# Optimization experiments

Hardware: AMD Instinct MI355X
Metric: run time of the kernel (lower is better)

Reference implementation:

```python
import jax, jax.numpy as jnp
import numpy as np

N, E, D, R, L, B, K = 10000, 160000, 256, 237, 6, 128, 33
EPS = 1e-6


def setup_inputs() -> dict:
    key = jax.random.key(0)
    ks = jax.random.split(key, 8)
    x = jax.random.uniform(ks[0], (N, D), dtype=jnp.float32)
    edge_index = jax.random.randint(ks[1], (2, E), 0, N)
    edge_type = jax.random.randint(ks[2], (E,), 0, R)
    batch = jax.random.randint(ks[3], (B, K, 3), 0, R)
    rel_embs = jax.random.normal(ks[4], (L, R, D), dtype=jnp.float32) * 0.02
    Ws = jax.random.normal(ks[5], (L, 13 * D, D), dtype=jnp.float32) * 0.02
    bs = jnp.zeros((L, D), dtype=jnp.float32)
    ln_scale = jnp.ones((L, D), dtype=jnp.float32)
    ln_bias = jnp.zeros((L, D), dtype=jnp.float32)
    relation_emb = jax.random.normal(ks[6], (R, D), dtype=jnp.float32) * 0.02
    return dict(x=x, rel_embs=rel_embs, Ws=Ws, bs=bs, ln_scale=ln_scale,
                ln_bias=ln_bias, relation_emb=relation_emb,
                edge_index=edge_index, edge_type=edge_type, batch=batch)


def _layer_norm(h, g, b, eps=1e-5):
    mu = jnp.mean(h, axis=-1, keepdims=True)
    var = jnp.var(h, axis=-1, keepdims=True)
    return (h - mu) * jax.lax.rsqrt(var + eps) * g + b


def _rgcn_conv(x, edge_index, edge_type, rel, W, b, g, be):
    # DistMult message + self-loop boundary, PNA aggregation, linear+LN+ReLU.
    n, d = x.shape
    src, dst = edge_index[0], edge_index[1]
    msg = x[src] * rel[edge_type]                       # [E, D]
    msg = jnp.concatenate([msg, x], axis=0)             # self-loop messages
    seg = jnp.concatenate([dst, jnp.arange(n)], axis=0)
    deg = jax.ops.segment_sum(jnp.ones((msg.shape[0],), jnp.float32), seg, n)  # >= 1
    inv_deg = 1.0 / deg[:, None]
    mean = jax.ops.segment_sum(msg, seg, n) * inv_deg
    sq_mean = jax.ops.segment_sum(msg * msg, seg, n) * inv_deg
    mx = jax.ops.segment_max(msg, seg, n)
    mn = jax.ops.segment_min(msg, seg, n)
    std = jnp.sqrt(jnp.clip(sq_mean - mean * mean, EPS))
    feats = jnp.concatenate([mean, mx, mn, std], axis=-1)          # [N, 4D]
    scale = jnp.log(deg)
    scale = scale / jnp.mean(scale)
    scales = jnp.stack([jnp.ones_like(scale), scale,
                        1.0 / jnp.clip(scale, 1e-2)], axis=-1)      # [N, 3]
    agg = (feats[:, :, None] * scales[:, None, :]).reshape(n, 12 * d)
    h = jnp.concatenate([agg, x], axis=-1) @ W + b                  # [N, D]
    return jax.nn.relu(_layer_norm(h, g, be))


def reference(x, rel_embs, Ws, bs, ln_scale, ln_bias, relation_emb,
              edge_index, edge_type, batch):
    for i in range(L):  # loop over layers (structurally distinct params)
        x = _rgcn_conv(x, edge_index, edge_type, rel_embs[i], Ws[i],
                       bs[i], ln_scale[i], ln_bias[i]) + x  # short_cut
    s = x[batch[:, :, 0]]                 # [B, K, D]
    r = relation_emb[batch[:, :, 1]]      # [B, K, D]
    t = x[batch[:, :, 2]]                 # [B, K, D]
    return jnp.sum(s * r * t, axis=-1)    # [B, K] DistMult scores
```

## Files before the change

kernel.cpp:

```cpp
#include <hip/hip_runtime.h>
#include <math.h>

typedef __attribute__((ext_vector_type(8))) _Float16 half8;
typedef __attribute__((ext_vector_type(4))) _Float16 half4;
typedef __attribute__((ext_vector_type(4))) float    floatx4;

#define N_NODES 10000
#define M_PAD   10112
#define MTILES  79
#define E_EDGES 160000
#define DIM     256
#define R_REL   237
#define L_LAYERS 6
#define B_BATCH 128
#define K_BATCH 33
#define K13     3328
#define KSPLIT  4
#define KSLICE  832
#define KS_STEPS 26
#define EPS_STD 1e-6f
#define EPS_LN  1e-5f

__device__ __forceinline__ void gload16(const void* g, void* lds) {
    __builtin_amdgcn_global_load_lds(
        (const __attribute__((address_space(1))) unsigned int*)g,
        (__attribute__((address_space(3))) unsigned int*)lds, 16, 0, 0);
}

__global__ void hist_kernel(const int* __restrict__ dst, int* __restrict__ deg) {
    int e = blockIdx.x * blockDim.x + threadIdx.x;
    if (e < E_EDGES) atomicAdd(&deg[dst[e]], 1);
}

__global__ void scan_kernel(const int* __restrict__ deg_in, int* __restrict__ offs,
                            int* __restrict__ cursor, float* __restrict__ sum_log) {
    __shared__ int   part[1024];
    __shared__ float slog[1024];
    int t = threadIdx.x;
    const int CH = 10;
    int base = t * CH;
    int lsum = 0; float ls = 0.f;
    for (int j = 0; j < CH; j++) {
        int i = base + j;
        if (i < N_NODES) { int d = deg_in[i]; lsum += d; ls += logf((float)(d + 1)); }
    }
    part[t] = lsum; slog[t] = ls;
    __syncthreads();
    for (int off = 1; off < 1024; off <<= 1) {
        int v = (t >= off) ? part[t - off] : 0;
        __syncthreads();
        part[t] += v;
        __syncthreads();
    }
    int run = part[t] - lsum;
    for (int j = 0; j < CH; j++) {
        int i = base + j;
        if (i < N_NODES) { offs[i] = run; cursor[i] = run; run += deg_in[i]; }
    }
    __syncthreads();
    for (int off = 512; off > 0; off >>= 1) {
        if (t < off) slog[t] += slog[t + off];
        __syncthreads();
    }
    if (t == 0) sum_log[0] = slog[0];
}

__global__ void fill_kernel(const int* __restrict__ src, const int* __restrict__ dst,
                            const int* __restrict__ et, int* __restrict__ cursor,
                            int* __restrict__ csr_src, int* __restrict__ csr_et) {
    int e = blockIdx.x * blockDim.x + threadIdx.x;
    if (e < E_EDGES) {
        int d = dst[e];
        int p = atomicAdd(&cursor[d], 1);
        csr_src[p] = src[e];
        csr_et[p]  = et[e];
    }
}

__global__ void scales_kernel(const int* __restrict__ deg_in, const float* __restrict__ sum_log,
                              float* __restrict__ s1, float* __restrict__ s2) {
    int i = blockIdx.x * blockDim.x + threadIdx.x;
    if (i < N_NODES) {
        float mean = sum_log[0] * (1.0f / (float)N_NODES);
        float sc = logf((float)(deg_in[i] + 1)) / mean;
        s1[i] = sc;
        s2[i] = 1.0f / fmaxf(sc, 0.01f);
    }
}

__global__ void wt_kernel(const float* __restrict__ Ws, _Float16* __restrict__ Wt) {
    int idx = blockIdx.x * 256 + threadIdx.x;
    const int TOT = L_LAYERS * 256 * K13;
    if (idx >= TOT) return;
    int l = idx / (256 * K13);
    int r = idx - l * (256 * K13);
    int n = r / K13, k = r - n * K13;
    int korig;
    if (k < 3072) {
        int t = k / 768;
        int rem = k - t * 768;
        int s = rem >> 8;
        int d = rem & 255;
        korig = (t * 256 + d) * 3 + s;
    } else {
        korig = k;
    }
    Wt[idx] = (_Float16)Ws[(size_t)l * K13 * 256 + (size_t)korig * 256 + n];
}

__global__ void cvt_kernel(const float* __restrict__ in, _Float16* __restrict__ outp, int n) {
    int i = blockIdx.x * 256 + threadIdx.x;
    if (i < n) outp[i] = (_Float16)in[i];
}

__global__ void agg_kernel(const float* __restrict__ x, const _Float16* __restrict__ xh,
                           const _Float16* __restrict__ relh,
                           const int* __restrict__ offs, const int* __restrict__ deg_in,
                           const int* __restrict__ csr_src, const int* __restrict__ csr_et,
                           _Float16* __restrict__ feats) {
    int wid  = threadIdx.x >> 6;
    int lane = threadIdx.x & 63;
    int node = blockIdx.x * 4 + wid;
    if (node >= N_NODES) return;
    int half = lane >> 5;
    int sub  = lane & 31;
    int off = offs[node];
    int end = off + deg_in[node];
    const half8* xh8 = (const half8*)xh;
    const half8* rh8 = (const half8*)relh;

    float s_[8], q_[8], mx_[8], mn_[8];
    #pragma unroll
    for (int i = 0; i < 8; i++) { s_[i] = 0.f; q_[i] = 0.f; mx_[i] = -INFINITY; mn_[i] = INFINITY; }

    for (int base = off; base < end; base += 2) {
        int e = base + half;
        if (e < end) {
            int sN = csr_src[e];
            int et = csr_et[e];
            half8 xv = xh8[(size_t)sN * 32 + sub];
            half8 rv = rh8[(size_t)et * 32 + sub];
            #pragma unroll
            for (int i = 0; i < 8; i++) {
                float m = (float)xv[i] * (float)rv[i];
                s_[i] += m; q_[i] += m * m;
                mx_[i] = fmaxf(mx_[i], m);
                mn_[i] = fminf(mn_[i], m);
            }
        }
    }
    #pragma unroll
    for (int i = 0; i < 8; i++) {
        s_[i] += __shfl_xor(s_[i], 32);
        q_[i] += __shfl_xor(q_[i], 32);
        mx_[i] = fmaxf(mx_[i], __shfl_xor(mx_[i], 32));
        mn_[i] = fminf(mn_[i], __shfl_xor(mn_[i], 32));
    }
    const float4* xrow = (const float4*)(x + (size_t)node * 256);
    float4 xa = xrow[sub * 2], xb = xrow[sub * 2 + 1];
    float xs[8] = {xa.x, xa.y, xa.z, xa.w, xb.x, xb.y, xb.z, xb.w};
    #pragma unroll
    for (int i = 0; i < 8; i++) {
        s_[i] += xs[i]; q_[i] += xs[i] * xs[i];
        mx_[i] = fmaxf(mx_[i], xs[i]);
        mn_[i] = fminf(mn_[i], xs[i]);
    }
    float inv = 1.0f / (float)(end - off + 1);
    half8 hm, hx, hn, hs;
    #pragma unroll
    for (int i = 0; i < 8; i++) {
        float mean = s_[i] * inv;
        float sd = sqrtf(fmaxf(q_[i] * inv - mean * mean, EPS_STD));
        hm[i] = (_Float16)mean; hx[i] = (_Float16)mx_[i];
        hn[i] = (_Float16)mn_[i]; hs[i] = (_Float16)sd;
    }
    half8* fout = (half8*)(feats + (size_t)node * 1024);
    if (half == 0) {
        fout[0 * 32 + sub] = hm;
        fout[1 * 32 + sub] = hx;
    } else {
        fout[2 * 32 + sub] = hn;
        fout[3 * 32 + sub] = hs;
    }
}

__launch_bounds__(256, 3)
__global__ void gemm_kernel(const _Float16* __restrict__ feats, const _Float16* __restrict__ xh,
                            const _Float16* __restrict__ Wt, const float* __restrict__ s1a,
                            const float* __restrict__ s2a, _Float16* __restrict__ hbuf) {
    __shared__ _Float16 sA[3][128 * 32];
    __shared__ _Float16 sB[3][128 * 32];

    int xcd = blockIdx.x & 7, loc = blockIdx.x >> 3;
    int lin = xcd * MTILES + loc;
    int ks  = lin / (2 * MTILES);
    int rem = lin - ks * (2 * MTILES);
    int nh  = rem / MTILES;
    int m   = rem - nh * MTILES;
    const int i0    = m * 128;
    const int n0    = nh * 128;
    const int kbase = ks * KSLICE;

    const int tid   = threadIdx.x;
    const int lane  = tid & 63;
    const int w     = tid >> 6;
    const int wr    = w >> 1;
    const int wc    = w & 1;
    const int row_l = lane & 15;
    const int kq    = lane >> 4;

    int a_off[4], b_off[4];
    #pragma unroll
    for (int rf = 0; rf < 4; rf++) {
        int r = wr * 64 + rf * 16 + row_l;
        a_off[rf] = r * 32 + ((kq ^ ((r >> 1) & 3)) & 3) * 8;
    }
    #pragma unroll
    for (int cf = 0; cf < 4; cf++) {
        int n_ = wc * 64 + cf * 16 + row_l;
        b_off[cf] = n_ * 32 + ((kq ^ ((n_ >> 1) & 3)) & 3) * 8;
    }

    const int arow = tid >> 2;
    const int ac   = tid & 3;
    const int aswz = ac ^ ((arow >> 1) & 3);
    const float s1lo = s1a[i0 + arow],      s2lo = s2a[i0 + arow];
    const float s1hi = s1a[i0 + arow + 64], s2hi = s2a[i0 + arow + 64];
    const _Float16* fb_lo = feats + (size_t)(i0 + arow) * 1024 + ac * 8;
    const _Float16* xb_lo = xh    + (size_t)(i0 + arow) * 256  + ac * 8;
    const _Float16* fb_hi = fb_lo + (size_t)64 * 1024;
    const _Float16* xb_hi = xb_lo + (size_t)64 * 256;

    const char* b_src[2];
    #pragma unroll
    for (int j = 0; j < 2; j++) {
        int rloc = j * 64 + w * 16 + (lane >> 2);
        int c = (lane & 3) ^ ((rloc >> 1) & 3);
        b_src[j] = (const char*)(Wt + (size_t)(n0 + rloc) * K13 + kbase + c * 8);
    }

    floatx4 acc[4][4];
    #pragma unroll
    for (int rf = 0; rf < 4; rf++)
        #pragma unroll
        for (int cf = 0; cf < 4; cf++)
            acc[rf][cf] = (floatx4){0.f, 0.f, 0.f, 0.f};

    half8 a0lo, a0hi, a1lo, a1hi, a2lo, a2hi;

#define A_OFS(S, OFS, SCL, SCH) do {                                          \
    int k0_ = kbase + (S) * 32;                                               \
    if (k0_ < 3072) {                                                         \
        int t_ = k0_ / 768;                                                   \
        int rem_ = k0_ - t_ * 768;                                            \
        int sI_ = rem_ >> 8;                                                  \
        OFS = t_ * 256 + (rem_ & 255);                                        \
        SCL = (sI_ == 0) ? 1.0f : (sI_ == 1 ? s1lo : s2lo);                   \
        SCH = (sI_ == 0) ? 1.0f : (sI_ == 1 ? s1hi : s2hi);                   \
    } else {                                                                  \
        OFS = -(k0_ - 3072) - 1;                                              \
        SCL = 1.0f; SCH = 1.0f;                                               \
    }                                                                         \
} while (0)

#define ALOAD(S, RLO, RHI) do {                                               \
    int ofs_; float scl_, sch_;                                               \
    A_OFS(S, ofs_, scl_, sch_);                                               \
    if (ofs_ >= 0) { RLO = *(const half8*)(fb_lo + ofs_);                     \
                     RHI = *(const half8*)(fb_hi + ofs_); }                   \
    else           { RLO = *(const half8*)(xb_lo + (-ofs_ - 1));              \
                     RHI = *(const half8*)(xb_hi + (-ofs_ - 1)); }            \
} while (0)

#define BSTAGE(BUF, S) do {                                                   \
    size_t koff_ = (size_t)(S) * 64;                                          \
    gload16(b_src[0] + koff_, (char*)(&sB[BUF][0]) + (0 * 64 + w * 16) * 64); \
    gload16(b_src[1] + koff_, (char*)(&sB[BUF][0]) + (1 * 64 + w * 16) * 64); \
} while (0)

#define AWRITE(BUF, S, RLO, RHI) do {                                         \
    int ofs_; float scl_, sch_;                                               \
    A_OFS(S, ofs_, scl_, sch_);                                               \
    half8 vl_ = RLO * (_Float16)scl_;                                         \
    half8 vh_ = RHI * (_Float16)sch_;                                         \
    *(half8*)(&sA[BUF][arow * 32 + aswz * 8]) = vl_;                          \
    *(half8*)(&sA[BUF][(arow + 64) * 32 + aswz * 8]) = vh_;                   \
} while (0)

#define COMPUTE(CB) do {                                                      \
    half8 af[4], bf[4];                                                       \
    _Pragma("unroll")                                                         \
    for (int rf = 0; rf < 4; rf++) af[rf] = *(const half8*)(&sA[CB][a_off[rf]]); \
    _Pragma("unroll")                                                         \
    for (int cf = 0; cf < 4; cf++) bf[cf] = *(const half8*)(&sB[CB][b_off[cf]]); \
    __builtin_amdgcn_s_setprio(1);                                            \
    _Pragma("unroll")                                                         \
    for (int rf = 0; rf < 4; rf++)                                            \
        _Pragma("unroll")                                                     \
        for (int cf = 0; cf < 4; cf++)                                        \
            acc[rf][cf] = __builtin_amdgcn_mfma_f32_16x16x32_f16(af[rf], bf[cf], acc[rf][cf], 0, 0, 0); \
    __builtin_amdgcn_s_setprio(0);                                            \
} while (0)

#define STEP(S, CBUF, ALO, AHI, NBUF, NLO, NHI) do {                          \
    asm volatile("s_waitcnt vmcnt(4)" ::: "memory");                          \
    AWRITE(CBUF, S, ALO, AHI);                                                \
    asm volatile("s_waitcnt lgkmcnt(0)" ::: "memory");                        \
    __builtin_amdgcn_sched_barrier(0);                                        \
    __builtin_amdgcn_s_barrier();                                             \
    ALOAD((S) + 2, NLO, NHI);                                                 \
    BSTAGE(NBUF, (S) + 2);                                                    \
    COMPUTE(CBUF);                                                            \
} while (0)

    ALOAD(0, a0lo, a0hi); BSTAGE(0, 0);
    ALOAD(1, a1lo, a1hi); BSTAGE(1, 1);

    int s = 0;
    for (int it = 0; it < 8; ++it, s += 3) {
        STEP(s + 0, 0, a0lo, a0hi, 2, a2lo, a2hi);
        STEP(s + 1, 1, a1lo, a1hi, 0, a0lo, a0hi);
        STEP(s + 2, 2, a2lo, a2hi, 1, a1lo, a1hi);
    }
    asm volatile("s_waitcnt vmcnt(4)" ::: "memory");
    AWRITE(0, 24, a0lo, a0hi);
    asm volatile("s_waitcnt lgkmcnt(0)" ::: "memory");
    __builtin_amdgcn_sched_barrier(0);
    __builtin_amdgcn_s_barrier();
    COMPUTE(0);
    asm volatile("s_waitcnt vmcnt(0)" ::: "memory");
    AWRITE(1, 25, a1lo, a1hi);
    asm volatile("s_waitcnt lgkmcnt(0)" ::: "memory");
    __builtin_amdgcn_sched_barrier(0);
    __builtin_amdgcn_s_barrier();
    COMPUTE(1);

#undef A_OFS
#undef ALOAD
#undef BSTAGE
#undef AWRITE
#undef COMPUTE
#undef STEP

    _Float16* outb = hbuf + (size_t)ks * M_PAD * 256;
    #pragma unroll
    for (int rf = 0; rf < 4; rf++) {
        #pragma unroll
        for (int j = 0; j < 4; j++) {
            int grow = i0 + wr * 64 + rf * 16 + kq * 4 + j;
            _Float16* orow = outb + (size_t)grow * 256 + n0 + wc * 64;
            #pragma unroll
            for (int cf = 0; cf < 4; cf++)
                orow[cf * 16 + row_l] = (_Float16)acc[rf][cf][j];
        }
    }
}

__global__ void ln_kernel(const _Float16* __restrict__ hbuf, const float* __restrict__ xin,
                          const float* __restrict__ bvec, const float* __restrict__ gvec,
                          const float* __restrict__ evec, float* __restrict__ xout,
                          _Float16* __restrict__ xhout) {
    int wid = threadIdx.x >> 6, lane = threadIdx.x & 63;
    int row = blockIdx.x * 4 + wid;
    if (row >= N_NODES) return;
    const half4* p0 = (const half4*)(hbuf + (size_t)row * 256);
    const half4* p1 = (const half4*)(hbuf + (size_t)M_PAD * 256     + (size_t)row * 256);
    const half4* p2 = (const half4*)(hbuf + (size_t)M_PAD * 256 * 2 + (size_t)row * 256);
    const half4* p3 = (const half4*)(hbuf + (size_t)M_PAD * 256 * 3 + (size_t)row * 256);
    half4 h0 = p0[lane], h1 = p1[lane], h2 = p2[lane], h3 = p3[lane];
    float4 bv = ((const float4*)bvec)[lane];
    float4 hv;
    hv.x = (float)h0.x + (float)h1.x + (float)h2.x + (float)h3.x + bv.x;
    hv.y = (float)h0.y + (float)h1.y + (float)h2.y + (float)h3.y + bv.y;
    hv.z = (float)h0.z + (float)h1.z + (float)h2.z + (float)h3.z + bv.z;
    hv.w = (float)h0.w + (float)h1.w + (float)h2.w + (float)h3.w + bv.w;
    float s = hv.x + hv.y + hv.z + hv.w;
    float qsq = hv.x*hv.x + hv.y*hv.y + hv.z*hv.z + hv.w*hv.w;
    #pragma unroll
    for (int off = 1; off < 64; off <<= 1) {
        s   += __shfl_xor(s, off);
        qsq += __shfl_xor(qsq, off);
    }
    float mu  = s * (1.0f / 256.0f);
    float var = qsq * (1.0f / 256.0f) - mu * mu;
    float rs  = rsqrtf(var + EPS_LN);
    float4 g = ((const float4*)gvec)[lane];
    float4 e = ((const float4*)evec)[lane];
    float4 xv = ((const float4*)(xin + (size_t)row * 256))[lane];
    float4 o;
    o.x = fmaxf((hv.x - mu) * rs * g.x + e.x, 0.f) + xv.x;
    o.y = fmaxf((hv.y - mu) * rs * g.y + e.y, 0.f) + xv.y;
    o.z = fmaxf((hv.z - mu) * rs * g.z + e.z, 0.f) + xv.z;
    o.w = fmaxf((hv.w - mu) * rs * g.w + e.w, 0.f) + xv.w;
    ((float4*)(xout + (size_t)row * 256))[lane] = o;
    half4 oh = { (_Float16)o.x, (_Float16)o.y, (_Float16)o.z, (_Float16)o.w };
    ((half4*)(xhout + (size_t)row * 256))[lane] = oh;
}

__global__ void score_kernel(const float* __restrict__ x, const float* __restrict__ remb,
                             const int* __restrict__ batch, float* __restrict__ out) {
    int wid = threadIdx.x >> 6, lane = threadIdx.x & 63;
    int g = blockIdx.x * 4 + wid;
    if (g >= B_BATCH * K_BATCH) return;
    int si = batch[g * 3 + 0], ri = batch[g * 3 + 1], ti = batch[g * 3 + 2];
    const float4* xs = (const float4*)(x + (size_t)si * 256);
    const float4* xr = (const float4*)(remb + (size_t)ri * 256);
    const float4* xt = (const float4*)(x + (size_t)ti * 256);
    float4 a = xs[lane], r = xr[lane], t = xt[lane];
    float p = a.x*r.x*t.x + a.y*r.y*t.y + a.z*r.z*t.z + a.w*r.w*t.w;
    #pragma unroll
    for (int off = 1; off < 64; off <<= 1) p += __shfl_xor(p, off);
    if (lane == 0) out[g] = p;
}

extern "C" void kernel_launch(void* const* d_in, const int* in_sizes, int n_in,
                              void* d_out, int out_size, void* d_ws, size_t ws_size,
                              hipStream_t stream) {
    const float* x_in     = (const float*)d_in[0];
    const float* rel_embs = (const float*)d_in[1];
    const float* Ws       = (const float*)d_in[2];
    const float* bs       = (const float*)d_in[3];
    const float* ln_s     = (const float*)d_in[4];
    const float* ln_b     = (const float*)d_in[5];
    const float* remb     = (const float*)d_in[6];
    const int*   eidx     = (const int*)d_in[7];
    const int*   etype    = (const int*)d_in[8];
    const int*   batch    = (const int*)d_in[9];
    float* out = (float*)d_out;

    char* wp = (char*)d_ws;
    size_t o = 0;
    auto alloc = [&](size_t bytes) { void* p = wp + o; o += (bytes + 255) & ~255ull; return p; };
    int*      deg_in  = (int*)     alloc((size_t)N_NODES * 4);
    int*      offs    = (int*)     alloc((size_t)N_NODES * 4);
    int*      cursor  = (int*)     alloc((size_t)N_NODES * 4);
    float*    s1      = (float*)   alloc((size_t)M_PAD * 4);
    float*    s2      = (float*)   alloc((size_t)M_PAD * 4);
    float*    sum_log = (float*)   alloc(256);
    int*      csr_src = (int*)     alloc((size_t)E_EDGES * 4);
    int*      csr_et  = (int*)     alloc((size_t)E_EDGES * 4);
    _Float16* feats   = (_Float16*)alloc((size_t)M_PAD * 1024 * 2);
    _Float16* Wt      = (_Float16*)alloc((size_t)L_LAYERS * 256 * K13 * 2);
    _Float16* hbuf    = (_Float16*)alloc((size_t)KSPLIT * M_PAD * 256 * 2);
    float*    xb0     = (float*)   alloc((size_t)M_PAD * 256 * 4);
    float*    xb1     = (float*)   alloc((size_t)M_PAD * 256 * 4);
    _Float16* xh0     = (_Float16*)alloc((size_t)M_PAD * 256 * 2);
    _Float16* xh1     = (_Float16*)alloc((size_t)M_PAD * 256 * 2);
    _Float16* relh    = (_Float16*)alloc((size_t)L_LAYERS * R_REL * 256 * 2);

    const int* src  = eidx;
    const int* dstp = eidx + E_EDGES;

    hipMemsetAsync(deg_in, 0, (size_t)N_NODES * 4, stream);
    hist_kernel<<<(E_EDGES + 255) / 256, 256, 0, stream>>>(dstp, deg_in);
    scan_kernel<<<1, 1024, 0, stream>>>(deg_in, offs, cursor, sum_log);
    fill_kernel<<<(E_EDGES + 255) / 256, 256, 0, stream>>>(src, dstp, etype, cursor, csr_src, csr_et);
    scales_kernel<<<(N_NODES + 255) / 256, 256, 0, stream>>>(deg_in, sum_log, s1, s2);
    {
        const int TOT = L_LAYERS * 256 * K13;
        wt_kernel<<<(TOT + 255) / 256, 256, 0, stream>>>(Ws, Wt);
        const int RT = L_LAYERS * R_REL * 256;
        cvt_kernel<<<(RT + 255) / 256, 256, 0, stream>>>(rel_embs, relh, RT);
        const int XT = N_NODES * 256;
        cvt_kernel<<<(XT + 255) / 256, 256, 0, stream>>>(x_in, xh0, XT);
    }
    hipMemcpyAsync(xb0, x_in, (size_t)N_NODES * 256 * 4, hipMemcpyDeviceToDevice, stream);

    float* xc = xb0; float* xn = xb1;
    _Float16* xhc = xh0; _Float16* xhn = xh1;
    for (int l = 0; l < L_LAYERS; l++) {
        agg_kernel<<<(N_NODES + 3) / 4, 256, 0, stream>>>(
            xc, xhc, relh + (size_t)l * R_REL * 256,
            offs, deg_in, csr_src, csr_et, feats);
        gemm_kernel<<<632, 256, 0, stream>>>(
            feats, xhc, Wt + (size_t)l * 256 * K13, s1, s2, hbuf);
        ln_kernel<<<(N_NODES + 3) / 4, 256, 0, stream>>>(
            hbuf, xc, bs + (size_t)l * 256, ln_s + (size_t)l * 256, ln_b + (size_t)l * 256, xn, xhn);
        float* t = xc; xc = xn; xn = t;
        _Float16* th = xhc; xhc = xhn; xhn = th;
    }
    score_kernel<<<(B_BATCH * K_BATCH + 3) / 4, 256, 0, stream>>>(xc, remb, batch, out);
}
```

Before: 505.6 us.

## Load GEMM A fragments directly into registers, bypassing LDS staging

The A operand of the split-K GEMM is no longer staged through a triple-buffered shared-memory tile. Each lane now loads its MFMA fragments straight from global memory in the per-lane layout and applies the degree scale in registers just before the MFMAs. This removes the LDS write, the LDS read and an lgkmcnt wait per K step, and frees shared memory for occupancy. The cost is four times more A register buffers and scattered 16-byte global loads, since each row is read by both column waves, and the vmcnt waits are retuned to match.

New measurement: 607.6 us. 20.2% more time.

```diff
diff --git a/kernel.cpp b/kernel.cpp
--- a/kernel.cpp
+++ b/kernel.cpp
@@ -188,7 +188,6 @@
 __global__ void gemm_kernel(const _Float16* __restrict__ feats, const _Float16* __restrict__ xh,
                             const _Float16* __restrict__ Wt, const float* __restrict__ s1a,
                             const float* __restrict__ s2a, _Float16* __restrict__ hbuf) {
-    __shared__ _Float16 sA[3][128 * 32];
     __shared__ _Float16 sB[3][128 * 32];
 
     int xcd = blockIdx.x & 7, loc = blockIdx.x >> 3;
@@ -209,27 +208,22 @@
     const int row_l = lane & 15;
     const int kq    = lane >> 4;
 
-    int a_off[4], b_off[4];
-    #pragma unroll
-    for (int rf = 0; rf < 4; rf++) {
-        int r = wr * 64 + rf * 16 + row_l;
-        a_off[rf] = r * 32 + ((kq ^ ((r >> 1) & 3)) & 3) * 8;
-    }
+    int b_off[4];
     #pragma unroll
     for (int cf = 0; cf < 4; cf++) {
         int n_ = wc * 64 + cf * 16 + row_l;
         b_off[cf] = n_ * 32 + ((kq ^ ((n_ >> 1) & 3)) & 3) * 8;
     }
 
-    const int arow = tid >> 2;
-    const int ac   = tid & 3;
-    const int aswz = ac ^ ((arow >> 1) & 3);
-    const float s1lo = s1a[i0 + arow],      s2lo = s2a[i0 + arow];
-    const float s1hi = s1a[i0 + arow + 64], s2hi = s2a[i0 + arow + 64];
-    const _Float16* fb_lo = feats + (size_t)(i0 + arow) * 1024 + ac * 8;
-    const _Float16* xb_lo = xh    + (size_t)(i0 + arow) * 256  + ac * 8;
-    const _Float16* fb_hi = fb_lo + (size_t)64 * 1024;
-    const _Float16* xb_hi = xb_lo + (size_t)64 * 256;
+    const int arow0 = i0 + wr * 64 + row_l;
+    const _Float16* pfeat = feats + (size_t)arow0 * 1024 + kq * 8;
+    const _Float16* pxh   = xh    + (size_t)arow0 * 256  + kq * 8;
+    float s1r[4], s2r[4];
+    #pragma unroll
+    for (int rf = 0; rf < 4; rf++) {
+        s1r[rf] = s1a[arow0 + rf * 16];
+        s2r[rf] = s2a[arow0 + rf * 16];
+    }
 
     const char* b_src[2];
     #pragma unroll
@@ -246,30 +240,24 @@
         for (int cf = 0; cf < 4; cf++)
             acc[rf][cf] = (floatx4){0.f, 0.f, 0.f, 0.f};
 
-    half8 a0lo, a0hi, a1lo, a1hi, a2lo, a2hi;
-
-#define A_OFS(S, OFS, SCL, SCH) do {                                          \
+    half8 a0[4], a1[4], a2[4];
+
+#define ALOADD(S, AR) do {                                                    \
     int k0_ = kbase + (S) * 32;                                               \
+    const _Float16* p_; int rs_;                                              \
     if (k0_ < 3072) {                                                         \
         int t_ = k0_ / 768;                                                   \
         int rem_ = k0_ - t_ * 768;                                            \
-        int sI_ = rem_ >> 8;                                                  \
-        OFS = t_ * 256 + (rem_ & 255);                                        \
-        SCL = (sI_ == 0) ? 1.0f : (sI_ == 1 ? s1lo : s2lo);                   \
-        SCH = (sI_ == 0) ? 1.0f : (sI_ == 1 ? s1hi : s2hi);                   \
+        p_ = pfeat + t_ * 256 + (rem_ & 255);                                 \
+        rs_ = 16 * 1024;                                                      \
     } else {                                                                  \
-        OFS = -(k0_ - 3072) - 1;                                              \
-        SCL = 1.0f; SCH = 1.0f;                                               \
+        p_ = pxh + (k0_ - 3072);                                              \
+        rs_ = 16 * 256;                                                       \
     }                                                                         \
-} while (0)
-
-#define ALOAD(S, RLO, RHI) do {                                               \
-    int ofs_; float scl_, sch_;                                               \
-    A_OFS(S, ofs_, scl_, sch_);                                               \
-    if (ofs_ >= 0) { RLO = *(const half8*)(fb_lo + ofs_);                     \
-                     RHI = *(const half8*)(fb_hi + ofs_); }                   \
-    else           { RLO = *(const half8*)(xb_lo + (-ofs_ - 1));              \
-                     RHI = *(const half8*)(xb_hi + (-ofs_ - 1)); }            \
+    AR[0] = *(const half8*)(p_);                                              \
+    AR[1] = *(const half8*)(p_ + rs_);                                        \
+    AR[2] = *(const half8*)(p_ + 2 * rs_);                                    \
+    AR[3] = *(const half8*)(p_ + 3 * rs_);                                    \
 } while (0)
 
 #define BSTAGE(BUF, S) do {                                                   \
@@ -278,21 +266,18 @@
     gload16(b_src[1] + koff_, (char*)(&sB[BUF][0]) + (1 * 64 + w * 16) * 64); \
 } while (0)
 
-#define AWRITE(BUF, S, RLO, RHI) do {                                         \
-    int ofs_; float scl_, sch_;                                               \
-    A_OFS(S, ofs_, scl_, sch_);                                               \
-    half8 vl_ = RLO * (_Float16)scl_;                                         \
-    half8 vh_ = RHI * (_Float16)sch_;                                         \
-    *(half8*)(&sA[BUF][arow * 32 + aswz * 8]) = vl_;                          \
-    *(half8*)(&sA[BUF][(arow + 64) * 32 + aswz * 8]) = vh_;                   \
-} while (0)
-
-#define COMPUTE(CB) do {                                                      \
-    half8 af[4], bf[4];                                                       \
-    _Pragma("unroll")                                                         \
-    for (int rf = 0; rf < 4; rf++) af[rf] = *(const half8*)(&sA[CB][a_off[rf]]); \
+#define COMPUTE(CB, S, AR) do {                                               \
+    int k0_ = kbase + (S) * 32;                                               \
+    int sI_ = 0;                                                              \
+    if (k0_ < 3072) { int rem_ = k0_ - (k0_ / 768) * 768; sI_ = rem_ >> 8; }  \
+    half8 bf[4], af[4];                                                       \
     _Pragma("unroll")                                                         \
     for (int cf = 0; cf < 4; cf++) bf[cf] = *(const half8*)(&sB[CB][b_off[cf]]); \
+    _Pragma("unroll")                                                         \
+    for (int rf = 0; rf < 4; rf++) {                                          \
+        float sc_ = (sI_ == 0) ? 1.0f : ((sI_ == 1) ? s1r[rf] : s2r[rf]);     \
+        af[rf] = AR[rf] * (_Float16)sc_;                                      \
+    }                                                                         \
     __builtin_amdgcn_s_setprio(1);                                            \
     _Pragma("unroll")                                                         \
     for (int rf = 0; rf < 4; rf++)                                            \
@@ -302,43 +287,32 @@
     __builtin_amdgcn_s_setprio(0);                                            \
 } while (0)
 
-#define STEP(S, CBUF, ALO, AHI, NBUF, NLO, NHI) do {                          \
-    asm volatile("s_waitcnt vmcnt(4)" ::: "memory");                          \
-    AWRITE(CBUF, S, ALO, AHI);                                                \
-    asm volatile("s_waitcnt lgkmcnt(0)" ::: "memory");                        \
-    __builtin_amdgcn_sched_barrier(0);                                        \
+#define STEP(S, CUR, ACUR, NXT, ANXT) do {                                    \
+    asm volatile("s_waitcnt vmcnt(6)" ::: "memory");                          \
     __builtin_amdgcn_s_barrier();                                             \
-    ALOAD((S) + 2, NLO, NHI);                                                 \
-    BSTAGE(NBUF, (S) + 2);                                                    \
-    COMPUTE(CBUF);                                                            \
+    ALOADD((S) + 2, ANXT);                                                    \
+    BSTAGE(NXT, (S) + 2);                                                     \
+    COMPUTE(CUR, S, ACUR);                                                    \
 } while (0)
 
-    ALOAD(0, a0lo, a0hi); BSTAGE(0, 0);
-    ALOAD(1, a1lo, a1hi); BSTAGE(1, 1);
+    ALOADD(0, a0); BSTAGE(0, 0);
+    ALOADD(1, a1); BSTAGE(1, 1);
 
     int s = 0;
     for (int it = 0; it < 8; ++it, s += 3) {
-        STEP(s + 0, 0, a0lo, a0hi, 2, a2lo, a2hi);
-        STEP(s + 1, 1, a1lo, a1hi, 0, a0lo, a0hi);
-        STEP(s + 2, 2, a2lo, a2hi, 1, a1lo, a1hi);
-    }
-    asm volatile("s_waitcnt vmcnt(4)" ::: "memory");
-    AWRITE(0, 24, a0lo, a0hi);
-    asm volatile("s_waitcnt lgkmcnt(0)" ::: "memory");
-    __builtin_amdgcn_sched_barrier(0);
+        STEP(s + 0, 0, a0, 2, a2);
+        STEP(s + 1, 1, a1, 0, a0);
+        STEP(s + 2, 2, a2, 1, a1);
+    }
+    asm volatile("s_waitcnt vmcnt(6)" ::: "memory");
     __builtin_amdgcn_s_barrier();
-    COMPUTE(0);
+    COMPUTE(0, 24, a0);
     asm volatile("s_waitcnt vmcnt(0)" ::: "memory");
-    AWRITE(1, 25, a1lo, a1hi);
-    asm volatile("s_waitcnt lgkmcnt(0)" ::: "memory");
-    __builtin_amdgcn_sched_barrier(0);
     __builtin_amdgcn_s_barrier();
-    COMPUTE(1);
-
-#undef A_OFS
-#undef ALOAD
+    COMPUTE(1, 25, a1);
+
+#undef ALOADD
 #undef BSTAGE
-#undef AWRITE
 #undef COMPUTE
 #undef STEP
 
```
